# Performance work log

Measured on AMD Instinct MI355X. Metric: run time of the kernel, lower is better.

The kernel has to match this reference:

```python
import jax, jax.numpy as jnp
import numpy as np


def setup_inputs() -> dict:
    key = jax.random.key(0)
    rain_hr = jax.random.normal(key, (16, 8, 1, 512, 512), dtype=jnp.float32)
    return {"rain_hr": rain_hr}


def reference(rain_hr):
    B, T, C, H, W = rain_hr.shape
    rain_mean = rain_hr.mean(axis=1)              # [B, C, H, W]

    fft = jnp.fft.fft2(rain_mean)                 # complex [B, C, H, W]
    power = jnp.abs(fft) ** 2                     # [B, C, H, W]

    # Integer radius map (torch: sqrt(...).long() truncates toward zero)
    ch, cw = H // 2, W // 2
    y = jnp.arange(H, dtype=jnp.float32) - ch
    x = jnp.arange(W, dtype=jnp.float32) - cw
    radius = jnp.sqrt(x[None, :] ** 2 + y[:, None] ** 2).astype(jnp.int32)  # [H, W]

    max_radius = min(H, W) // 2

    # power[..., mask].mean() == sum over (B, C, pixels at radius r) / (B*C*count_r)
    power_hw = power.sum(axis=(0, 1))             # [H, W]
    flat_r = radius.ravel()
    # out-of-range radii (>= max_radius) are dropped by segment_sum
    seg_sum = jax.ops.segment_sum(power_hw.ravel(), flat_r, num_segments=max_radius)
    counts = jax.ops.segment_sum(jnp.ones((H * W,), jnp.float32), flat_r, num_segments=max_radius)

    cnt = counts[1:]                               # radii 1 .. max_radius-1
    denom = jnp.maximum(cnt, 1.0) * (B * C)
    gen_spectrum = jnp.where(cnt > 0, seg_sum[1:] / denom, 0.0)

    k = jnp.arange(1, max_radius, dtype=jnp.float32)
    ref = k ** (-5.0 / 3.0)
    ref = ref / (ref.sum() + 1e-8)

    gen_norm = gen_spectrum / (gen_spectrum.sum() + 1e-8)
    loss = jnp.mean((gen_norm - ref) ** 2)
    return loss
```

## Files before the change

### kernel.cpp

```cpp
#include <hip/hip_runtime.h>
#include <math.h>

#define N 512
#define PLANE ((size_t)N * N)
#define NEG2PI (-6.28318530717958647692f)

__device__ inline void dft8(float (&xr)[8], float (&xi)[8]) {
    const float S = 0.70710678118654752440f;
    float t0r = xr[0] + xr[4], t0i = xi[0] + xi[4];
    float t4r = xr[0] - xr[4], t4i = xi[0] - xi[4];
    float t1r = xr[1] + xr[5], t1i = xi[1] + xi[5];
    float t5r = xr[1] - xr[5], t5i = xi[1] - xi[5];
    float t2r = xr[2] + xr[6], t2i = xi[2] + xi[6];
    float t6r = xr[2] - xr[6], t6i = xi[2] - xi[6];
    float t3r = xr[3] + xr[7], t3i = xi[3] + xi[7];
    float t7r = xr[3] - xr[7], t7i = xi[3] - xi[7];
    float o1r = S * (t5r + t5i), o1i = S * (t5i - t5r);
    float o2r = t6i,             o2i = -t6r;
    float o3r = S * (t7i - t7r), o3i = -S * (t7r + t7i);
    float p0r = t0r + t2r, p0i = t0i + t2i;
    float p1r = t1r + t3r, p1i = t1i + t3i;
    float q0r = t0r - t2r, q0i = t0i - t2i;
    float q1r = t1i - t3i, q1i = -(t1r - t3r);
    xr[0] = p0r + p1r; xi[0] = p0i + p1i;
    xr[4] = p0r - p1r; xi[4] = p0i - p1i;
    xr[2] = q0r + q1r; xi[2] = q0i + q1i;
    xr[6] = q0r - q1r; xi[6] = q0i - q1i;
    float r0r = t4r + o2r, r0i = t4i + o2i;
    float r1r = o1r + o3r, r1i = o1i + o3i;
    float u0r = t4r - o2r, u0i = t4i - o2i;
    float u1r = o1i - o3i, u1i = -(o1r - o3r);
    xr[1] = r0r + r1r; xi[1] = r0i + r1i;
    xr[5] = r0r - r1r; xi[5] = r0i - r1i;
    xr[3] = u0r + u1r; xi[3] = u0i + u1i;
    xr[7] = u0r - u1r; xi[7] = u0i - u1i;
}

__device__ inline void twiddle_apply(float (&xr)[8], float (&xi)[8], float ang1) {
    float ts, tc;
    __sincosf(ang1, &ts, &tc);
    float wr = tc, wi = ts;
    #pragma unroll
    for (int k = 1; k < 8; ++k) {
        float nr = xr[k] * wr - xi[k] * wi;
        float ni = xr[k] * wi + xi[k] * wr;
        xr[k] = nr; xi[k] = ni;
        float w2r = wr * tc - wi * ts;
        float w2i = wr * ts + wi * tc;
        wr = w2r; wi = w2i;
    }
}

__device__ inline void fft512_wave(float (&xr)[8], float (&xi)[8],
                                   float* sre, float* sim, const int l) {
    dft8(xr, xi);
    twiddle_apply(xr, xi, (NEG2PI / 512.0f) * (float)l);
    const int w0 = l + (l >> 3);
    #pragma unroll
    for (int k = 0; k < 8; ++k) { sre[72 * k + w0] = xr[k]; sim[72 * k + w0] = xi[k]; }
    const int i2 = l & 7;
    const int rbase = 72 * (l >> 3) + i2;
    #pragma unroll
    for (int q = 0; q < 8; ++q) { xr[q] = sre[rbase + 9 * q]; xi[q] = sim[rbase + 9 * q]; }
    dft8(xr, xi);
    twiddle_apply(xr, xi, (NEG2PI / 64.0f) * (float)i2);
    #pragma unroll
    for (int k = 0; k < 8; ++k) { sre[rbase + 9 * k] = xr[k]; sim[rbase + 9 * k] = xi[k]; }
    const int r3 = 9 * l;
    #pragma unroll
    for (int q = 0; q < 8; ++q) { xr[q] = sre[r3 + q]; xi[q] = sim[r3 + q]; }
    dft8(xr, xi);
}

__device__ inline int freq_of(int k, int l) {
    return 64 * k + 8 * (l & 7) + (l >> 3);
}

__global__ __launch_bounds__(256, 4) void kern_rowfft(const float* __restrict__ in,
                                                      float2* __restrict__ ws) {
    __shared__ float sRe[4][576];
    __shared__ float sIm[4][576];
    const int wv = threadIdx.x >> 6;
    const int l  = threadIdx.x & 63;
    const int y  = blockIdx.x * 4 + wv;
    const int j  = blockIdx.y;
    const float* baseA = in + ((size_t)j * 8) * PLANE + (size_t)y * N;
    const float* baseB = in + ((size_t)(j + 8) * 8) * PLANE + (size_t)y * N;
    float xr[8], xi[8];
    #pragma unroll
    for (int q = 0; q < 8; ++q) {
        const int xp = l + 64 * q;
        float sa = 0.f, sb = 0.f;
        #pragma unroll
        for (int tt = 0; tt < 8; ++tt) {
            sa += baseA[tt * PLANE + xp];
            sb += baseB[tt * PLANE + xp];
        }
        xr[q] = sa * 0.125f;
        xi[q] = sb * 0.125f;
    }
    fft512_wave(xr, xi, sRe[wv], sIm[wv], l);
    float2* wp = ws + ((size_t)j << 18) + y;
    #pragma unroll
    for (int k = 0; k < 8; ++k) {
        wp[(size_t)freq_of(k, l) << 9] = make_float2(xr[k], xi[k]);
    }
}

__global__ __launch_bounds__(256, 4) void kern_colfft(const float2* __restrict__ ws,
                                                      float* __restrict__ gseg,
                                                      float* __restrict__ gcnt) {
    __shared__ float sRe[4][576];
    __shared__ float sIm[4][576];
    __shared__ float lseg[256];
    __shared__ float lcnt[256];
    const int wv = threadIdx.x >> 6;
    const int l  = threadIdx.x & 63;
    const int fx = blockIdx.x * 4 + wv;
    const int j  = blockIdx.y;
    lseg[threadIdx.x] = 0.f;
    lcnt[threadIdx.x] = 0.f;
    __syncthreads();
    const float2* cp = ws + ((size_t)j << 18) + ((size_t)fx << 9);
    float xr[8], xi[8];
    #pragma unroll
    for (int q = 0; q < 8; ++q) {
        float2 v = cp[l + 64 * q];
        xr[q] = v.x; xi[q] = v.y;
    }
    fft512_wave(xr, xi, sRe[wv], sIm[wv], l);
    const int dx = fx - 256;
    const int dx2 = dx * dx;
    #pragma unroll
    for (int k = 0; k < 8; ++k) {
        const int fy = freq_of(k, l);
        const int dy = fy - 256;
        const int d2 = dx2 + dy * dy;
        int r = (int)sqrtf((float)d2);
        if ((r + 1) * (r + 1) <= d2) r++;
        else if (r * r > d2) r--;
        if (r >= 1 && r < 256) {
            atomicAdd(&lseg[r], xr[k] * xr[k] + xi[k] * xi[k]);
            if (j == 0) atomicAdd(&lcnt[r], 1.0f);
        }
    }
    __syncthreads();
    const int t = threadIdx.x;
    if (lseg[t] != 0.f) atomicAdd(&gseg[j * 256 + t], lseg[t]);
    if (j == 0 && lcnt[t] != 0.f) atomicAdd(&gcnt[t], lcnt[t]);
}

__global__ __launch_bounds__(256) void kern_loss(const float* __restrict__ gseg,
                                                 const float* __restrict__ gcnt,
                                                 float* __restrict__ out) {
    __shared__ float red[256];
    const int t = threadIdx.x;
    float gen = 0.f, refv = 0.f;
    if (t >= 1) {
        float s = 0.f;
        #pragma unroll
        for (int j = 0; j < 8; ++j) s += gseg[j * 256 + t];
        float c = gcnt[t];
        gen  = (c > 0.f) ? s / (fmaxf(c, 1.f) * 16.0f) : 0.f;
        refv = powf((float)t, -5.0f / 3.0f);
    }
    red[t] = gen; __syncthreads();
    for (int off = 128; off > 0; off >>= 1) {
        if (t < off) red[t] += red[t + off];
        __syncthreads();
    }
    const float sgen = red[0]; __syncthreads();
    red[t] = refv; __syncthreads();
    for (int off = 128; off > 0; off >>= 1) {
        if (t < off) red[t] += red[t + off];
        __syncthreads();
    }
    const float sref = red[0]; __syncthreads();
    const float gn = gen  / (sgen + 1e-8f);
    const float rn = refv / (sref + 1e-8f);
    red[t] = (gn - rn) * (gn - rn); __syncthreads();
    for (int off = 128; off > 0; off >>= 1) {
        if (t < off) red[t] += red[t + off];
        __syncthreads();
    }
    if (t == 0) out[0] = red[0] / 255.0f;
}

extern "C" void kernel_launch(void* const* d_in, const int* in_sizes, int n_in,
                              void* d_out, int out_size, void* d_ws, size_t ws_size,
                              hipStream_t stream) {
    const float* in = (const float*)d_in[0];
    float2* planes = (float2*)d_ws;
    float* bins = (float*)((char*)d_ws + (size_t)8 * N * N * sizeof(float2));
    float* gseg = bins;
    float* gcnt = bins + 8 * 256;
    hipMemsetAsync(bins, 0, (8 * 256 + 256) * sizeof(float), stream);
    kern_rowfft<<<dim3(128, 8), 256, 0, stream>>>(in, planes);
    kern_colfft<<<dim3(128, 8), 256, 0, stream>>>(planes, gseg, gcnt);
    kern_loss<<<1, 256, 0, stream>>>(gseg, gcnt, (float*)d_out);
}
```

Before: 225.9 us.

## Store row-FFT output row-major and transpose column tiles through LDS

After: 216.8 us. 1.04x faster.

```diff
diff --git a/kernel.cpp b/kernel.cpp
--- a/kernel.cpp
+++ b/kernel.cpp
@@ -72,10 +72,6 @@
     dft8(xr, xi);
 }
 
-__device__ inline int freq_of(int k, int l) {
-    return 64 * k + 8 * (l & 7) + (l >> 3);
-}
-
 __global__ __launch_bounds__(256, 4) void kern_rowfft(const float* __restrict__ in,
                                                       float2* __restrict__ ws) {
     __shared__ float sRe[4][576];
@@ -86,54 +82,77 @@
     const int j  = blockIdx.y;
     const float* baseA = in + ((size_t)j * 8) * PLANE + (size_t)y * N;
     const float* baseB = in + ((size_t)(j + 8) * 8) * PLANE + (size_t)y * N;
-    float xr[8], xi[8];
-    #pragma unroll
-    for (int q = 0; q < 8; ++q) {
-        const int xp = l + 64 * q;
-        float sa = 0.f, sb = 0.f;
+    float* re = sRe[wv];
+    float* im = sIm[wv];
+    #pragma unroll
+    for (int c0 = 0; c0 < 2; ++c0) {
+        const int c = l + 64 * c0;
+        float4 sa = make_float4(0.f, 0.f, 0.f, 0.f);
+        float4 sb = make_float4(0.f, 0.f, 0.f, 0.f);
         #pragma unroll
         for (int tt = 0; tt < 8; ++tt) {
-            sa += baseA[tt * PLANE + xp];
-            sb += baseB[tt * PLANE + xp];
+            float4 a = *(const float4*)(baseA + tt * PLANE + 4 * c);
+            float4 b = *(const float4*)(baseB + tt * PLANE + 4 * c);
+            sa.x += a.x; sa.y += a.y; sa.z += a.z; sa.w += a.w;
+            sb.x += b.x; sb.y += b.y; sb.z += b.z; sb.w += b.w;
         }
-        xr[q] = sa * 0.125f;
-        xi[q] = sb * 0.125f;
-    }
-    fft512_wave(xr, xi, sRe[wv], sIm[wv], l);
-    float2* wp = ws + ((size_t)j << 18) + y;
+        const int i0 = 4 * c;
+        const int p0 = i0 + (i0 >> 3);
+        re[p0 + 0] = sa.x * 0.125f; re[p0 + 1] = sa.y * 0.125f;
+        re[p0 + 2] = sa.z * 0.125f; re[p0 + 3] = sa.w * 0.125f;
+        im[p0 + 0] = sb.x * 0.125f; im[p0 + 1] = sb.y * 0.125f;
+        im[p0 + 2] = sb.z * 0.125f; im[p0 + 3] = sb.w * 0.125f;
+    }
+    float xr[8], xi[8];
+    #pragma unroll
+    for (int q = 0; q < 8; ++q) {
+        const int p = l + (l >> 3) + 72 * q;
+        xr[q] = re[p]; xi[q] = im[p];
+    }
+    fft512_wave(xr, xi, re, im, l);
+    float2* wp = ws + ((size_t)j << 18) + ((size_t)y << 9);
     #pragma unroll
     for (int k = 0; k < 8; ++k) {
-        wp[(size_t)freq_of(k, l) << 9] = make_float2(xr[k], xi[k]);
-    }
-}
-
-__global__ __launch_bounds__(256, 4) void kern_colfft(const float2* __restrict__ ws,
+        wp[64 * k + 8 * (l & 7) + (l >> 3)] = make_float2(xr[k], xi[k]);
+    }
+}
+
+__global__ __launch_bounds__(512, 4) void kern_colfft(const float2* __restrict__ ws,
                                                       float* __restrict__ gseg,
                                                       float* __restrict__ gcnt) {
-    __shared__ float sRe[4][576];
-    __shared__ float sIm[4][576];
+    __shared__ float sA[8 * 576];
+    __shared__ float sB[8 * 576];
     __shared__ float lseg[256];
     __shared__ float lcnt[256];
-    const int wv = threadIdx.x >> 6;
-    const int l  = threadIdx.x & 63;
-    const int fx = blockIdx.x * 4 + wv;
-    const int j  = blockIdx.y;
-    lseg[threadIdx.x] = 0.f;
-    lcnt[threadIdx.x] = 0.f;
+    const int w   = threadIdx.x >> 6;
+    const int l   = threadIdx.x & 63;
+    const int fx0 = blockIdx.x * 8;
+    const int j   = blockIdx.y;
+    if (threadIdx.x < 256) { lseg[threadIdx.x] = 0.f; lcnt[threadIdx.x] = 0.f; }
+    const float2* base = ws + ((size_t)j << 18) + fx0;
+    #pragma unroll
+    for (int i = 0; i < 8; ++i) {
+        const int y = (w << 6) + (i << 3) + (l >> 3);
+        const int f = l & 7;
+        float2 v = base[((size_t)y << 9) + f];
+        sA[y * 9 + f] = v.x;
+        sB[y * 9 + f] = v.y;
+    }
     __syncthreads();
-    const float2* cp = ws + ((size_t)j << 18) + ((size_t)fx << 9);
     float xr[8], xi[8];
     #pragma unroll
     for (int q = 0; q < 8; ++q) {
-        float2 v = cp[l + 64 * q];
-        xr[q] = v.x; xi[q] = v.y;
-    }
-    fft512_wave(xr, xi, sRe[wv], sIm[wv], l);
-    const int dx = fx - 256;
+        const int y = l + (q << 6);
+        xr[q] = sA[y * 9 + w];
+        xi[q] = sB[y * 9 + w];
+    }
+    __syncthreads();
+    fft512_wave(xr, xi, sA + w * 576, sB + w * 576, l);
+    const int dx  = fx0 + w - 256;
     const int dx2 = dx * dx;
     #pragma unroll
     for (int k = 0; k < 8; ++k) {
-        const int fy = freq_of(k, l);
+        const int fy = 64 * k + 8 * (l & 7) + (l >> 3);
         const int dy = fy - 256;
         const int d2 = dx2 + dy * dy;
         int r = (int)sqrtf((float)d2);
@@ -146,8 +165,11 @@
     }
     __syncthreads();
     const int t = threadIdx.x;
-    if (lseg[t] != 0.f) atomicAdd(&gseg[j * 256 + t], lseg[t]);
-    if (j == 0 && lcnt[t] != 0.f) atomicAdd(&gcnt[t], lcnt[t]);
+    if (t < 256) {
+        if (lseg[t] != 0.f) atomicAdd(&gseg[j * 256 + t], lseg[t]);
+    } else if (j == 0) {
+        if (lcnt[t - 256] != 0.f) atomicAdd(&gcnt[t - 256], lcnt[t - 256]);
+    }
 }
 
 __global__ __launch_bounds__(256) void kern_loss(const float* __restrict__ gseg,
@@ -196,6 +218,6 @@
     float* gcnt = bins + 8 * 256;
     hipMemsetAsync(bins, 0, (8 * 256 + 256) * sizeof(float), stream);
     kern_rowfft<<<dim3(128, 8), 256, 0, stream>>>(in, planes);
-    kern_colfft<<<dim3(128, 8), 256, 0, stream>>>(planes, gseg, gcnt);
+    kern_colfft<<<dim3(64, 8), 512, 0, stream>>>(planes, gseg, gcnt);
     kern_loss<<<1, 256, 0, stream>>>(gseg, gcnt, (float*)d_out);
 }
```
